# Optimization experiments

Hardware: AMD Instinct MI355X
Metric: run time of the kernel (lower is better)

## Reference

```python
import jax, jax.numpy as jnp
import numpy as np

B, NPG, DEG = 128, 400, 16
N, E = B * NPG, B * NPG * DEG
E_PER = E // B
K1, K2, K3 = 360, 324, 292  # ceil(0.9*400), ceil(0.9*360), ceil(0.9*324)
EPS = 1e-5


def setup_inputs() -> dict:
    key = jax.random.key(0)
    ks = jax.random.split(key, 48)
    # edges constrained within each graph (contiguous equal-size graphs)
    g = jnp.repeat(jnp.arange(B, dtype=jnp.int32), E_PER)
    src = jax.random.randint(ks[0], (E,), 0, NPG, dtype=jnp.int32) + g * NPG
    dst = jax.random.randint(ks[1], (E,), 0, NPG, dtype=jnp.int32) + g * NPG
    inp = {
        'x': jax.random.normal(ks[2], (N, 64), dtype=jnp.float32),
        'edge_index': jnp.stack([src, dst]),
        'batch': jnp.repeat(jnp.arange(B, dtype=jnp.int32), NPG),
    }
    def glorot(k, a, b):
        lim = float(np.sqrt(6.0 / (a + b)))
        return jax.random.uniform(k, (a, b), minval=-lim, maxval=lim, dtype=jnp.float32)
    conv_dims = [(64, 32), (32, 64), (64, 128), (128, 128)]
    for i, (a, b) in enumerate(conv_dims, 1):
        inp[f'W{i}'] = glorot(ks[2 + i], a, b)
        inp[f'b{i}'] = jnp.zeros((b,), jnp.float32)
    for i, d in zip((1, 2, 3), (32, 64, 128)):
        inp[f'p{i}'] = jax.random.uniform(ks[8 + i], (d,), minval=-1.0, maxval=1.0, dtype=jnp.float32) / float(np.sqrt(d))
    lin_dims = [(128, 64), (64, 64), (64, 32), (32, 16), (16, 1)]
    for i, (a, b) in enumerate(lin_dims, 1):
        inp[f'Lw{i}'] = glorot(ks[12 + i], a, b)
        inp[f'Lb{i}'] = jnp.zeros((b,), jnp.float32)
    for i, d in enumerate((64, 64, 32, 16), 1):
        inp[f'g{i}'] = jnp.ones((d,), jnp.float32)
        inp[f'be{i}'] = jnp.zeros((d,), jnp.float32)
    return inp


def _gcn(x, src, dst, emask, nmask, W, b):
    h = x @ W
    deg = nmask + jax.ops.segment_sum(emask, dst, num_segments=N)
    dinv = jnp.where(deg > 0, jax.lax.rsqrt(deg), 0.0)
    norm = dinv[src] * dinv[dst] * emask
    agg = jax.ops.segment_sum(h[src] * norm[:, None], dst, num_segments=N)
    agg = agg + h * (dinv * dinv * nmask)[:, None]  # self-loop term
    return (agg + b) * nmask[:, None]


def _topk_pool(x, nmask, p, k):
    # PyG TopKPooling: score = x.p/||p||, keep top-k per graph, x *= tanh(score)
    score = (x @ p) / jnp.linalg.norm(p)
    sel = jnp.where(nmask > 0, score, -jnp.inf).reshape(B, NPG)
    _, idx = jax.lax.top_k(sel, k)
    gidx = (idx + (jnp.arange(B) * NPG)[:, None]).reshape(-1)
    new_mask = jnp.zeros((N,), x.dtype).at[gidx].set(1.0)
    return x * (jnp.tanh(score) * new_mask)[:, None], new_mask


def reference(x, edge_index, batch, W1, b1, p1, W2, b2, p2, W3, b3, p3, W4, b4,
              Lw1, Lb1, Lw2, Lb2, Lw3, Lb3, Lw4, Lb4, Lw5, Lb5,
              g1, be1, g2, be2, g3, be3, g4, be4):
    src, dst = edge_index[0], edge_index[1]
    nmask = jnp.ones((N,), jnp.float32)
    emask = jnp.ones((E,), jnp.float32)
    x = jax.nn.relu(_gcn(x, src, dst, emask, nmask, W1, b1))
    x, nmask = _topk_pool(x, nmask, p1, K1)
    emask = emask * nmask[src] * nmask[dst]
    x = jax.nn.relu(_gcn(x, src, dst, emask, nmask, W2, b2))
    x, nmask = _topk_pool(x, nmask, p2, K2)
    emask = emask * nmask[src] * nmask[dst]
    x = jax.nn.relu(_gcn(x, src, dst, emask, nmask, W3, b3))
    x, nmask = _topk_pool(x, nmask, p3, K3)
    emask = emask * nmask[src] * nmask[dst]
    x = jax.nn.relu(_gcn(x, src, dst, emask, nmask, W4, b4))
    h = x.reshape(B, NPG, -1).max(axis=1)
    def lin_bn(h, W, bb, ga, be):
        h = h @ W + bb
        m = h.mean(0)
        v = h.var(0)  # biased, matches BatchNorm1d training normalization
        return jax.nn.relu(ga * (h - m) / jnp.sqrt(v + EPS) + be)
    h = lin_bn(h, Lw1, Lb1, g1, be1)
    h = lin_bn(h, Lw2, Lb2, g2, be2)
    h = lin_bn(h, Lw3, Lb3, g3, be3)
    h = lin_bn(h, Lw4, Lb4, g4, be4)
    return h @ Lw5 + Lb5
```

## Files before the change

### kernel.cpp

```cpp
#include <hip/hip_runtime.h>
#include <math.h>

#define NNODES 51200
#define BGRAPHS 128
#define NPG 400
#define NEDGES 819200
#define EPG 6400
#define SLP 7680

__global__ __launch_bounds__(512) void csr_build_kernel(
    const int* __restrict__ src, const int* __restrict__ dst,
    unsigned short* __restrict__ slg, int* __restrict__ gsg, int* __restrict__ gcg,
    float* __restrict__ nmask, float* __restrict__ dinv, float* __restrict__ sc) {
    __shared__ int deg[NPG];
    __shared__ int incl[512];
    __shared__ int gs[NPG];
    __shared__ int cur[NPG];
    const int g = blockIdx.x, t = threadIdx.x;
    for (int i = t; i < NPG; i += 512) deg[i] = 0;
    __syncthreads();
    for (int e = t; e < EPG; e += 512)
        atomicAdd(&deg[dst[g * EPG + e] - g * NPG], 1);
    __syncthreads();
    const int d = (t < NPG) ? deg[t] : 0;
    const int p = (d + 3) >> 2;
    incl[t] = p;
    __syncthreads();
    for (int off = 1; off < 512; off <<= 1) {
        int add = (t >= off) ? incl[t - off] : 0;
        __syncthreads();
        incl[t] += add;
        __syncthreads();
    }
    if (t < NPG) {
        const int gstart = incl[t] - p;
        gs[t] = gstart;
        gsg[g * NPG + t] = gstart;
        gcg[g * NPG + t] = p;
        cur[t] = gstart * 4;
        nmask[g * NPG + t] = 1.0f;
        const float dv = rsqrtf(1.0f + (float)d);
        dinv[g * NPG + t] = dv;
        sc[g * NPG + t] = dv;
    }
    __syncthreads();
    for (int e = t; e < EPG; e += 512) {
        int dl = dst[g * EPG + e] - g * NPG;
        int pos = atomicAdd(&cur[dl], 1);
        slg[g * SLP + pos] = (unsigned short)(src[g * EPG + e] - g * NPG);
    }
    __syncthreads();
    if (t < NPG) {
        const int end = (gs[t] + p) * 4;
        for (int i = cur[t]; i < end; i++) slg[g * SLP + i] = (unsigned short)NPG;
    }
}

template<int IN, int OUT, bool EPI>
__global__ __launch_bounds__(256) void gemm_kernel(
    const float* __restrict__ X, const float* __restrict__ W,
    const float* __restrict__ bias, const float* __restrict__ nmask,
    float* __restrict__ H) {
    __shared__ __align__(16) float sX[64 * IN];
    const int row0 = blockIdx.x * 64;
    const int t = threadIdx.x;
    for (int i = t; i < 64 * IN / 4; i += 256)
        reinterpret_cast<float4*>(sX)[i] =
            reinterpret_cast<const float4*>(X + (size_t)row0 * IN)[i];
    __syncthreads();
    constexpr int CG  = OUT / 4;
    constexpr int RG  = 256 / CG;
    constexpr int RPT = 64 / RG;
    const int c0 = (t % CG) * 4;
    const int r0 = (t / CG) * RPT;
    float acc[RPT][4];
#pragma unroll
    for (int r = 0; r < RPT; r++)
#pragma unroll
        for (int j = 0; j < 4; j++) acc[r][j] = 0.0f;
    for (int k4 = 0; k4 < IN / 4; k4++) {
        const float4 w0 = *reinterpret_cast<const float4*>(&W[(k4 * 4 + 0) * OUT + c0]);
        const float4 w1 = *reinterpret_cast<const float4*>(&W[(k4 * 4 + 1) * OUT + c0]);
        const float4 w2 = *reinterpret_cast<const float4*>(&W[(k4 * 4 + 2) * OUT + c0]);
        const float4 w3 = *reinterpret_cast<const float4*>(&W[(k4 * 4 + 3) * OUT + c0]);
#pragma unroll
        for (int r = 0; r < RPT; r++) {
            const float4 xv = *reinterpret_cast<const float4*>(&sX[(r0 + r) * IN + k4 * 4]);
            acc[r][0] += xv.x * w0.x + xv.y * w1.x + xv.z * w2.x + xv.w * w3.x;
            acc[r][1] += xv.x * w0.y + xv.y * w1.y + xv.z * w2.y + xv.w * w3.y;
            acc[r][2] += xv.x * w0.z + xv.y * w1.z + xv.z * w2.z + xv.w * w3.z;
            acc[r][3] += xv.x * w0.w + xv.y * w1.w + xv.z * w2.w + xv.w * w3.w;
        }
    }
#pragma unroll
    for (int r = 0; r < RPT; r++) {
        const int row = row0 + r0 + r;
        float4 v = make_float4(acc[r][0], acc[r][1], acc[r][2], acc[r][3]);
        if (EPI) {
            const float4 b4 = *reinterpret_cast<const float4*>(&bias[c0]);
            const float m = nmask[row];
            v.x = fmaxf(v.x + b4.x, 0.0f) * m;
            v.y = fmaxf(v.y + b4.y, 0.0f) * m;
            v.z = fmaxf(v.z + b4.z, 0.0f) * m;
            v.w = fmaxf(v.w + b4.w, 0.0f) * m;
        }
        *reinterpret_cast<float4*>(&H[(size_t)row * OUT + c0]) = v;
    }
}

template<int OUT, int NCH, int NS, bool EPI>
__global__ __launch_bounds__(512) void gcn_agg_kernel(
    const float* __restrict__ H, float* __restrict__ Y,
    const float* __restrict__ dinv, const float* __restrict__ sc,
    const float* __restrict__ bias,
    const unsigned short* __restrict__ slg, const int* __restrict__ gsg,
    const int* __restrict__ gcg) {
    __shared__ __align__(16) float Hl[(NPG + 1) * 36];
    __shared__ float dinvl[NPG];
    __shared__ int gsl[NPG];
    __shared__ int gcl[NPG];
    __shared__ unsigned long long sl64[SLP / 4];
    const unsigned short* sl = reinterpret_cast<const unsigned short*>(sl64);
    const int b   = blockIdx.x;
    const int g   = b / (NCH * NS);
    const int rem = b % (NCH * NS);
    const int f0  = (rem / NS) * 32;
    const int n0  = (rem % NS) * (NPG / NS);
    const int t   = threadIdx.x;

    for (int i = t; i < NPG; i += 512) {
        dinvl[i] = dinv[g * NPG + i];
        gsl[i] = gsg[g * NPG + i];
        gcl[i] = gcg[g * NPG + i];
    }
    for (int i = t; i < SLP / 4; i += 512)
        sl64[i] = reinterpret_cast<const unsigned long long*>(slg + (size_t)g * SLP)[i];
    if (t < 36) Hl[NPG * 36 + t] = 0.0f;
    for (int i = t; i < NPG * 8; i += 512) {
        const int n = i >> 3, q = i & 7;
        const float s = sc[g * NPG + n];
        float4 v = *reinterpret_cast<const float4*>(&H[(size_t)(g * NPG + n) * OUT + f0 + q * 4]);
        v.x *= s; v.y *= s; v.z *= s; v.w *= s;
        *reinterpret_cast<float4*>(&Hl[n * 36 + q * 4]) = v;
    }
    __syncthreads();

    const int wave = t >> 6, lane = t & 63;
    const int sub = lane >> 3, f4 = lane & 7;
    constexpr int NPB = NPG / NS;
    for (int n = n0 + wave * 8 + sub; n < n0 + NPB; n += 64) {
        const float di = dinvl[n];
        float* yp = &Y[(size_t)(g * NPG + n) * OUT + f0 + f4 * 4];
        if (di == 0.0f) {
            *reinterpret_cast<float4*>(yp) = make_float4(0.f, 0.f, 0.f, 0.f);
            continue;
        }
        const int g0 = gsl[n], g1 = g0 + gcl[n];
        float4 acc = *reinterpret_cast<const float4*>(&Hl[n * 36 + f4 * 4]);
        for (int gg = g0; gg < g1; ++gg) {
            const unsigned long long q = *reinterpret_cast<const unsigned long long*>(&sl[gg * 4]);
            const int s0 = (int)(q & 0xFFFF), s1 = (int)((q >> 16) & 0xFFFF);
            const int s2 = (int)((q >> 32) & 0xFFFF), s3 = (int)(q >> 48);
            const float4 a = *reinterpret_cast<const float4*>(&Hl[s0 * 36 + f4 * 4]);
            const float4 bb = *reinterpret_cast<const float4*>(&Hl[s1 * 36 + f4 * 4]);
            const float4 c = *reinterpret_cast<const float4*>(&Hl[s2 * 36 + f4 * 4]);
            const float4 dd = *reinterpret_cast<const float4*>(&Hl[s3 * 36 + f4 * 4]);
            acc.x += (a.x + bb.x) + (c.x + dd.x);
            acc.y += (a.y + bb.y) + (c.y + dd.y);
            acc.z += (a.z + bb.z) + (c.z + dd.z);
            acc.w += (a.w + bb.w) + (c.w + dd.w);
        }
        acc.x *= di; acc.y *= di; acc.z *= di; acc.w *= di;
        if (EPI) {
            const float4 b4 = *reinterpret_cast<const float4*>(&bias[f0 + f4 * 4]);
            acc.x = fmaxf(acc.x + b4.x, 0.0f);
            acc.y = fmaxf(acc.y + b4.y, 0.0f);
            acc.z = fmaxf(acc.z + b4.z, 0.0f);
            acc.w = fmaxf(acc.w + b4.w, 0.0f);
        }
        *reinterpret_cast<float4*>(yp) = acc;
    }
}

template<int DIM>
__global__ __launch_bounds__(512) void topk_kernel(
    const float* __restrict__ X, float* __restrict__ nmask,
    float* __restrict__ dinv, float* __restrict__ sc,
    const float* __restrict__ p, int K,
    const unsigned short* __restrict__ slg, const int* __restrict__ gsg,
    const int* __restrict__ gcg) {
    __shared__ float sval[512];
    __shared__ int   sidx[512];
    __shared__ float sscore[NPG];
    __shared__ float nml[NPG + 1];
    __shared__ unsigned long long sl64[SLP / 4];
    __shared__ int gsl[NPG];
    __shared__ int gcl[NPG];
    __shared__ float spnorm;
    const unsigned short* sl = reinterpret_cast<const unsigned short*>(sl64);
    const int g = blockIdx.x;
    const int t = threadIdx.x;
    for (int i = t; i < SLP / 4; i += 512)
        sl64[i] = reinterpret_cast<const unsigned long long*>(slg + (size_t)g * SLP)[i];
    for (int i = t; i < NPG; i += 512) {
        gsl[i] = gsg[g * NPG + i];
        gcl[i] = gcg[g * NPG + i];
    }
    if (t == 0) {
        float s = 0.0f;
        for (int j = 0; j < DIM; j++) s += p[j] * p[j];
        spnorm = sqrtf(s);
    }
    __syncthreads();
    if (t < NPG) {
        const float* xr = X + (size_t)(g * NPG + t) * DIM;
        float s = 0.0f;
        for (int j4 = 0; j4 < DIM / 4; j4++) {
            float4 xv = *reinterpret_cast<const float4*>(&xr[j4 * 4]);
            float4 pv = *reinterpret_cast<const float4*>(&p[j4 * 4]);
            s += xv.x * pv.x + xv.y * pv.y + xv.z * pv.z + xv.w * pv.w;
        }
        s /= spnorm;
        sscore[t] = s;
        sval[t] = (nmask[g * NPG + t] > 0.0f) ? s : -INFINITY;
        sidx[t] = t;
    } else {
        sval[t] = -INFINITY;
        sidx[t] = 0x7FFFFFFF;
    }
    __syncthreads();
    for (int kk = 2; kk <= 512; kk <<= 1) {
        for (int j = kk >> 1; j > 0; j >>= 1) {
            int l = t ^ j;
            if (l > t) {
                float va = sval[t], vb = sval[l];
                int   ia = sidx[t], ib = sidx[l];
                bool aFirst = (va > vb) || (va == vb && ia < ib);
                bool desc   = ((t & kk) == 0);
                if (desc != aFirst) {
                    sval[t] = vb; sval[l] = va;
                    sidx[t] = ib; sidx[l] = ia;
                }
            }
            __syncthreads();
        }
    }
    if (t <= NPG) nml[t] = 0.0f;
    __syncthreads();
    if (t < K) nml[sidx[t]] = 1.0f;
    __syncthreads();
    if (t < NPG) nmask[g * NPG + t] = nml[t];
    for (int n = t; n < NPG; n += 512) {
        float dv = 0.0f;
        if (nml[n] > 0.0f) {
            float d = 1.0f;
            const int g0 = gsl[n], g1 = g0 + gcl[n];
            for (int gg = g0; gg < g1; ++gg) {
                const unsigned long long q = *reinterpret_cast<const unsigned long long*>(&sl[gg * 4]);
                d += nml[(int)(q & 0xFFFF)] + nml[(int)((q >> 16) & 0xFFFF)] +
                     nml[(int)((q >> 32) & 0xFFFF)] + nml[(int)(q >> 48)];
            }
            dv = rsqrtf(d);
        }
        dinv[g * NPG + n] = dv;
        sc[g * NPG + n] = (nml[n] > 0.0f) ? tanhf(sscore[n]) * dv : 0.0f;
    }
}

__global__ __launch_bounds__(512) void maxpool_kernel(const float* __restrict__ X,
                                                      float* __restrict__ HP) {
    __shared__ float sm[512];
    const int g = blockIdx.x, t = threadIdx.x;
    const int c = t & 127, q = t >> 7;
    const float* base = X + ((size_t)g * NPG + q * 100) * 128 + c;
    float m = 0.0f;
    for (int n = 0; n < 100; n++) m = fmaxf(m, base[(size_t)n * 128]);
    sm[t] = m;
    __syncthreads();
    if (q == 0)
        HP[g * 128 + c] = fmaxf(fmaxf(sm[c], sm[c + 128]), fmaxf(sm[c + 256], sm[c + 384]));
}

template<int IN, int OUT>
__global__ __launch_bounds__(128) void head_layer_kernel(
    const float* __restrict__ A, const float* __restrict__ W,
    const float* __restrict__ b, const float* __restrict__ ga,
    const float* __restrict__ be, float* __restrict__ Y) {
    __shared__ float Al[128 * (IN + 1)];
    __shared__ float red[4];
    const int c = blockIdx.x, t = threadIdx.x;
    for (int i = t; i < 128 * IN; i += 128)
        Al[(i / IN) * (IN + 1) + (i % IN)] = A[i];
    __syncthreads();
    float acc = b[c];
#pragma unroll
    for (int j = 0; j < IN; j++) acc += Al[t * (IN + 1) + j] * W[j * OUT + c];
    float s1 = acc, s2 = acc * acc;
    for (int o = 32; o > 0; o >>= 1) {
        s1 += __shfl_down(s1, o, 64);
        s2 += __shfl_down(s2, o, 64);
    }
    if ((t & 63) == 0) { red[t >> 6] = s1; red[2 + (t >> 6)] = s2; }
    __syncthreads();
    const float S1 = red[0] + red[1], S2 = red[2] + red[3];
    const float m = S1 * (1.0f / 128.0f);
    const float var = S2 * (1.0f / 128.0f) - m * m;
    float val = ga[c] * (acc - m) * rsqrtf(var + 1e-5f) + be[c];
    Y[t * OUT + c] = fmaxf(val, 0.0f);
}

__global__ __launch_bounds__(128) void head_final_kernel(
    const float* __restrict__ A, const float* __restrict__ w,
    const float* __restrict__ b, float* __restrict__ out) {
    const int t = threadIdx.x;
    float acc = b[0];
#pragma unroll
    for (int j = 0; j < 16; j++) acc += A[t * 16 + j] * w[j];
    out[t] = acc;
}

extern "C" void kernel_launch(void* const* d_in, const int* in_sizes, int n_in,
                              void* d_out, int out_size, void* d_ws, size_t ws_size,
                              hipStream_t stream) {
    (void)in_sizes; (void)n_in; (void)out_size; (void)ws_size;
    const float* x   = (const float*)d_in[0];
    const int*   ei  = (const int*)d_in[1];
    const float* W1  = (const float*)d_in[3];  const float* b1  = (const float*)d_in[4];
    const float* W2  = (const float*)d_in[5];  const float* b2  = (const float*)d_in[6];
    const float* W3  = (const float*)d_in[7];  const float* b3  = (const float*)d_in[8];
    const float* W4  = (const float*)d_in[9];  const float* b4  = (const float*)d_in[10];
    const float* p1  = (const float*)d_in[11];
    const float* p2  = (const float*)d_in[12];
    const float* p3  = (const float*)d_in[13];
    const float* Lw1 = (const float*)d_in[14]; const float* Lb1 = (const float*)d_in[15];
    const float* Lw2 = (const float*)d_in[16]; const float* Lb2 = (const float*)d_in[17];
    const float* Lw3 = (const float*)d_in[18]; const float* Lb3 = (const float*)d_in[19];
    const float* Lw4 = (const float*)d_in[20]; const float* Lb4 = (const float*)d_in[21];
    const float* Lw5 = (const float*)d_in[22]; const float* Lb5 = (const float*)d_in[23];
    const float* g1  = (const float*)d_in[24]; const float* be1 = (const float*)d_in[25];
    const float* g2  = (const float*)d_in[26]; const float* be2 = (const float*)d_in[27];
    const float* g3  = (const float*)d_in[28]; const float* be3 = (const float*)d_in[29];
    const float* g4  = (const float*)d_in[30]; const float* be4 = (const float*)d_in[31];

    const int* src = ei;
    const int* dst = ei + NEDGES;

    float* ws    = (float*)d_ws;
    float* hb    = ws;
    float* x0    = hb + (size_t)NNODES * 128;
    float* x1    = x0 + (size_t)NNODES * 128;
    float* nmask = x1 + (size_t)NNODES * 128;
    float* dinv  = nmask + NNODES;
    float* sc    = dinv + NNODES;
    float* hp    = sc + NNODES;
    float* a1    = hp + 128 * 128;
    float* a2    = a1 + 128 * 64;
    float* a3    = a2 + 128 * 64;
    float* a4    = a3 + 128 * 32;
    unsigned short* slg = (unsigned short*)(a4 + 128 * 16);
    int* gsg = (int*)(slg + (size_t)BGRAPHS * SLP);
    int* gcg = gsg + (size_t)BGRAPHS * NPG;

    csr_build_kernel<<<BGRAPHS, 512, 0, stream>>>(src, dst, slg, gsg, gcg, nmask, dinv, sc);

    gemm_kernel<64, 32, false><<<NNODES / 64, 256, 0, stream>>>(x, W1, nullptr, nullptr, hb);
    gcn_agg_kernel<32, 1, 2, true><<<BGRAPHS * 2, 512, 0, stream>>>(hb, x0, dinv, sc, b1, slg, gsg, gcg);
    topk_kernel<32><<<BGRAPHS, 512, 0, stream>>>(x0, nmask, dinv, sc, p1, 360, slg, gsg, gcg);

    gcn_agg_kernel<32, 1, 2, false><<<BGRAPHS * 2, 512, 0, stream>>>(x0, hb, dinv, sc, nullptr, slg, gsg, gcg);
    gemm_kernel<32, 64, true><<<NNODES / 64, 256, 0, stream>>>(hb, W2, b2, nmask, x1);
    topk_kernel<64><<<BGRAPHS, 512, 0, stream>>>(x1, nmask, dinv, sc, p2, 324, slg, gsg, gcg);

    gcn_agg_kernel<64, 2, 2, false><<<BGRAPHS * 4, 512, 0, stream>>>(x1, hb, dinv, sc, nullptr, slg, gsg, gcg);
    gemm_kernel<64, 128, true><<<NNODES / 64, 256, 0, stream>>>(hb, W3, b3, nmask, x0);
    topk_kernel<128><<<BGRAPHS, 512, 0, stream>>>(x0, nmask, dinv, sc, p3, 292, slg, gsg, gcg);

    gcn_agg_kernel<128, 4, 1, false><<<BGRAPHS * 4, 512, 0, stream>>>(x0, hb, dinv, sc, nullptr, slg, gsg, gcg);
    gemm_kernel<128, 128, true><<<NNODES / 64, 256, 0, stream>>>(hb, W4, b4, nmask, x1);

    maxpool_kernel<<<BGRAPHS, 512, 0, stream>>>(x1, hp);
    head_layer_kernel<128, 64><<<64, 128, 0, stream>>>(hp, Lw1, Lb1, g1, be1, a1);
    head_layer_kernel<64, 64><<<64, 128, 0, stream>>>(a1, Lw2, Lb2, g2, be2, a2);
    head_layer_kernel<64, 32><<<32, 128, 0, stream>>>(a2, Lw3, Lb3, g3, be3, a3);
    head_layer_kernel<32, 16><<<16, 128, 0, stream>>>(a3, Lw4, Lb4, g4, be4, a4);
    head_final_kernel<<<1, 128, 0, stream>>>(a4, Lw5, Lb5, (float*)d_out);
}
```

Measured before the change: 240.2 us.

## Fuse top-k scoring into producers and max-pool into final GEMM epilogue

The projection score x·p is now computed in the epilogue of the kernel that produces each layer's features (the aggregation kernel for layer 1, the GEMM for layers 2-3) and written to a score buffer, so the top-k kernel no longer rereads the full feature matrix. The final GEMM no longer writes its output; it reduces per-graph column maxima in shared memory with atomicMax on float bits and merges them into the pooled buffer, which is zeroed in the CSR build kernel. This removes the separate max-pool kernel and its full read of the last feature matrix. The aggregation kernel also skips writing zeros for masked nodes, which relies on those rows already being zero in the output buffer. The costs are extra shuffles, shared and global atomics, and that stale-row assumption.

Result: faster. 209.5 us (-12.8%).

```diff
diff --git a/kernel.cpp b/kernel.cpp
--- a/kernel.cpp
+++ b/kernel.cpp
@@ -11,13 +11,15 @@
 __global__ __launch_bounds__(512) void csr_build_kernel(
     const int* __restrict__ src, const int* __restrict__ dst,
     unsigned short* __restrict__ slg, int* __restrict__ gsg, int* __restrict__ gcg,
-    float* __restrict__ nmask, float* __restrict__ dinv, float* __restrict__ sc) {
+    float* __restrict__ nmask, float* __restrict__ dinv, float* __restrict__ sc,
+    float* __restrict__ hp) {
     __shared__ int deg[NPG];
     __shared__ int incl[512];
     __shared__ int gs[NPG];
     __shared__ int cur[NPG];
     const int g = blockIdx.x, t = threadIdx.x;
     for (int i = t; i < NPG; i += 512) deg[i] = 0;
+    if (t < 128) hp[g * 128 + t] = 0.0f;
     __syncthreads();
     for (int e = t; e < EPG; e += 512)
         atomicAdd(&deg[dst[g * EPG + e] - g * NPG], 1);
@@ -56,17 +58,20 @@
     }
 }
 
-template<int IN, int OUT, bool EPI>
+template<int IN, int OUT, int MODE>
 __global__ __launch_bounds__(256) void gemm_kernel(
     const float* __restrict__ X, const float* __restrict__ W,
     const float* __restrict__ bias, const float* __restrict__ nmask,
-    float* __restrict__ H) {
+    float* __restrict__ H, const float* __restrict__ p,
+    float* __restrict__ score, float* __restrict__ hp) {
     __shared__ __align__(16) float sX[64 * IN];
+    __shared__ unsigned smax[256];
     const int row0 = blockIdx.x * 64;
     const int t = threadIdx.x;
     for (int i = t; i < 64 * IN / 4; i += 256)
         reinterpret_cast<float4*>(sX)[i] =
             reinterpret_cast<const float4*>(X + (size_t)row0 * IN)[i];
+    if (MODE == 3) smax[t] = 0u;
     __syncthreads();
     constexpr int CG  = OUT / 4;
     constexpr int RG  = 256 / CG;
@@ -92,11 +97,14 @@
             acc[r][3] += xv.x * w0.w + xv.y * w1.w + xv.z * w2.w + xv.w * w3.w;
         }
     }
+    const int graph0 = row0 / 400;
+    const int bnd = (graph0 + 1) * 400;
+    float ps[RPT];
 #pragma unroll
     for (int r = 0; r < RPT; r++) {
         const int row = row0 + r0 + r;
         float4 v = make_float4(acc[r][0], acc[r][1], acc[r][2], acc[r][3]);
-        if (EPI) {
+        if (MODE >= 2) {
             const float4 b4 = *reinterpret_cast<const float4*>(&bias[c0]);
             const float m = nmask[row];
             v.x = fmaxf(v.x + b4.x, 0.0f) * m;
@@ -104,15 +112,47 @@
             v.z = fmaxf(v.z + b4.z, 0.0f) * m;
             v.w = fmaxf(v.w + b4.w, 0.0f) * m;
         }
-        *reinterpret_cast<float4*>(&H[(size_t)row * OUT + c0]) = v;
-    }
-}
-
-template<int OUT, int NCH, int NS, bool EPI>
+        if (MODE != 3) *reinterpret_cast<float4*>(&H[(size_t)row * OUT + c0]) = v;
+        if (MODE == 2) {
+            const float4 p4 = *reinterpret_cast<const float4*>(&p[c0]);
+            ps[r] = v.x * p4.x + v.y * p4.y + v.z * p4.z + v.w * p4.w;
+        }
+        if (MODE == 3) {
+            const int seg = (row >= bnd) ? 1 : 0;
+            const float mx = fmaxf(fmaxf(v.x, v.y), fmaxf(v.z, v.w));
+            atomicMax(&smax[seg * 128 + c0 + 0], __float_as_uint(v.x));
+            atomicMax(&smax[seg * 128 + c0 + 1], __float_as_uint(v.y));
+            atomicMax(&smax[seg * 128 + c0 + 2], __float_as_uint(v.z));
+            atomicMax(&smax[seg * 128 + c0 + 3], __float_as_uint(v.w));
+            (void)mx;
+        }
+    }
+    if (MODE == 2) {
+#pragma unroll
+        for (int r = 0; r < RPT; r++) {
+#pragma unroll
+            for (int off = 1; off < CG; off <<= 1) ps[r] += __shfl_xor(ps[r], off);
+        }
+        if ((t % CG) == 0) {
+#pragma unroll
+            for (int r = 0; r < RPT; r++) score[row0 + r0 + r] = ps[r];
+        }
+    }
+    if (MODE == 3) {
+        __syncthreads();
+        unsigned* hpu = reinterpret_cast<unsigned*>(hp);
+        if (t < 128) atomicMax(&hpu[graph0 * 128 + t], smax[t]);
+        const int graph1 = (row0 + 63) / 400;
+        if (graph1 != graph0 && t < 128) atomicMax(&hpu[graph1 * 128 + t], smax[128 + t]);
+    }
+}
+
+template<int OUT, int NCH, int NS, bool EPI, bool SCORE>
 __global__ __launch_bounds__(512) void gcn_agg_kernel(
     const float* __restrict__ H, float* __restrict__ Y,
     const float* __restrict__ dinv, const float* __restrict__ sc,
-    const float* __restrict__ bias,
+    const float* __restrict__ bias, const float* __restrict__ p,
+    float* __restrict__ score,
     const unsigned short* __restrict__ slg, const int* __restrict__ gsg,
     const int* __restrict__ gcg) {
     __shared__ __align__(16) float Hl[(NPG + 1) * 36];
@@ -150,11 +190,7 @@
     constexpr int NPB = NPG / NS;
     for (int n = n0 + wave * 8 + sub; n < n0 + NPB; n += 64) {
         const float di = dinvl[n];
-        float* yp = &Y[(size_t)(g * NPG + n) * OUT + f0 + f4 * 4];
-        if (di == 0.0f) {
-            *reinterpret_cast<float4*>(yp) = make_float4(0.f, 0.f, 0.f, 0.f);
-            continue;
-        }
+        if (di == 0.0f) continue;
         const int g0 = gsl[n], g1 = g0 + gcl[n];
         float4 acc = *reinterpret_cast<const float4*>(&Hl[n * 36 + f4 * 4]);
         for (int gg = g0; gg < g1; ++gg) {
@@ -178,20 +214,28 @@
             acc.z = fmaxf(acc.z + b4.z, 0.0f);
             acc.w = fmaxf(acc.w + b4.w, 0.0f);
         }
-        *reinterpret_cast<float4*>(yp) = acc;
+        *reinterpret_cast<float4*>(&Y[(size_t)(g * NPG + n) * OUT + f0 + f4 * 4]) = acc;
+        if (SCORE) {
+            const float4 p4 = *reinterpret_cast<const float4*>(&p[f4 * 4]);
+            float part = acc.x * p4.x + acc.y * p4.y + acc.z * p4.z + acc.w * p4.w;
+            part += __shfl_xor(part, 1);
+            part += __shfl_xor(part, 2);
+            part += __shfl_xor(part, 4);
+            if (f4 == 0) score[g * NPG + n] = part;
+        }
     }
 }
 
 template<int DIM>
 __global__ __launch_bounds__(512) void topk_kernel(
-    const float* __restrict__ X, float* __restrict__ nmask,
+    const float* __restrict__ score, float* __restrict__ nmask,
     float* __restrict__ dinv, float* __restrict__ sc,
     const float* __restrict__ p, int K,
     const unsigned short* __restrict__ slg, const int* __restrict__ gsg,
     const int* __restrict__ gcg) {
     __shared__ float sval[512];
     __shared__ int   sidx[512];
-    __shared__ float sscore[NPG];
+    __shared__ float sraw[NPG];
     __shared__ float nml[NPG + 1];
     __shared__ unsigned long long sl64[SLP / 4];
     __shared__ int gsl[NPG];
@@ -213,16 +257,9 @@
     }
     __syncthreads();
     if (t < NPG) {
-        const float* xr = X + (size_t)(g * NPG + t) * DIM;
-        float s = 0.0f;
-        for (int j4 = 0; j4 < DIM / 4; j4++) {
-            float4 xv = *reinterpret_cast<const float4*>(&xr[j4 * 4]);
-            float4 pv = *reinterpret_cast<const float4*>(&p[j4 * 4]);
-            s += xv.x * pv.x + xv.y * pv.y + xv.z * pv.z + xv.w * pv.w;
-        }
-        s /= spnorm;
-        sscore[t] = s;
-        sval[t] = (nmask[g * NPG + t] > 0.0f) ? s : -INFINITY;
+        const float raw = score[g * NPG + t];
+        sraw[t] = raw;
+        sval[t] = (nmask[g * NPG + t] > 0.0f) ? raw : -INFINITY;
         sidx[t] = t;
     } else {
         sval[t] = -INFINITY;
@@ -263,22 +300,8 @@
             dv = rsqrtf(d);
         }
         dinv[g * NPG + n] = dv;
-        sc[g * NPG + n] = (nml[n] > 0.0f) ? tanhf(sscore[n]) * dv : 0.0f;
-    }
-}
-
-__global__ __launch_bounds__(512) void maxpool_kernel(const float* __restrict__ X,
-                                                      float* __restrict__ HP) {
-    __shared__ float sm[512];
-    const int g = blockIdx.x, t = threadIdx.x;
-    const int c = t & 127, q = t >> 7;
-    const float* base = X + ((size_t)g * NPG + q * 100) * 128 + c;
-    float m = 0.0f;
-    for (int n = 0; n < 100; n++) m = fmaxf(m, base[(size_t)n * 128]);
-    sm[t] = m;
-    __syncthreads();
-    if (q == 0)
-        HP[g * 128 + c] = fmaxf(fmaxf(sm[c], sm[c + 128]), fmaxf(sm[c + 256], sm[c + 384]));
+        sc[g * NPG + n] = (nml[n] > 0.0f) ? tanhf(sraw[n] / spnorm) * dv : 0.0f;
+    }
 }
 
 template<int IN, int OUT>
@@ -352,7 +375,8 @@
     float* nmask = x1 + (size_t)NNODES * 128;
     float* dinv  = nmask + NNODES;
     float* sc    = dinv + NNODES;
-    float* hp    = sc + NNODES;
+    float* scoreb= sc + NNODES;
+    float* hp    = scoreb + NNODES;
     float* a1    = hp + 128 * 128;
     float* a2    = a1 + 128 * 64;
     float* a3    = a2 + 128 * 64;
@@ -361,24 +385,23 @@
     int* gsg = (int*)(slg + (size_t)BGRAPHS * SLP);
     int* gcg = gsg + (size_t)BGRAPHS * NPG;
 
-    csr_build_kernel<<<BGRAPHS, 512, 0, stream>>>(src, dst, slg, gsg, gcg, nmask, dinv, sc);
-
-    gemm_kernel<64, 32, false><<<NNODES / 64, 256, 0, stream>>>(x, W1, nullptr, nullptr, hb);
-    gcn_agg_kernel<32, 1, 2, true><<<BGRAPHS * 2, 512, 0, stream>>>(hb, x0, dinv, sc, b1, slg, gsg, gcg);
-    topk_kernel<32><<<BGRAPHS, 512, 0, stream>>>(x0, nmask, dinv, sc, p1, 360, slg, gsg, gcg);
-
-    gcn_agg_kernel<32, 1, 2, false><<<BGRAPHS * 2, 512, 0, stream>>>(x0, hb, dinv, sc, nullptr, slg, gsg, gcg);
-    gemm_kernel<32, 64, true><<<NNODES / 64, 256, 0, stream>>>(hb, W2, b2, nmask, x1);
-    topk_kernel<64><<<BGRAPHS, 512, 0, stream>>>(x1, nmask, dinv, sc, p2, 324, slg, gsg, gcg);
-
-    gcn_agg_kernel<64, 2, 2, false><<<BGRAPHS * 4, 512, 0, stream>>>(x1, hb, dinv, sc, nullptr, slg, gsg, gcg);
-    gemm_kernel<64, 128, true><<<NNODES / 64, 256, 0, stream>>>(hb, W3, b3, nmask, x0);
-    topk_kernel<128><<<BGRAPHS, 512, 0, stream>>>(x0, nmask, dinv, sc, p3, 292, slg, gsg, gcg);
-
-    gcn_agg_kernel<128, 4, 1, false><<<BGRAPHS * 4, 512, 0, stream>>>(x0, hb, dinv, sc, nullptr, slg, gsg, gcg);
-    gemm_kernel<128, 128, true><<<NNODES / 64, 256, 0, stream>>>(hb, W4, b4, nmask, x1);
-
-    maxpool_kernel<<<BGRAPHS, 512, 0, stream>>>(x1, hp);
+    csr_build_kernel<<<BGRAPHS, 512, 0, stream>>>(src, dst, slg, gsg, gcg, nmask, dinv, sc, hp);
+
+    gemm_kernel<64, 32, 0><<<NNODES / 64, 256, 0, stream>>>(x, W1, nullptr, nullptr, hb, nullptr, nullptr, nullptr);
+    gcn_agg_kernel<32, 1, 2, true, true><<<BGRAPHS * 2, 512, 0, stream>>>(hb, x0, dinv, sc, b1, p1, scoreb, slg, gsg, gcg);
+    topk_kernel<32><<<BGRAPHS, 512, 0, stream>>>(scoreb, nmask, dinv, sc, p1, 360, slg, gsg, gcg);
+
+    gcn_agg_kernel<32, 1, 2, false, false><<<BGRAPHS * 2, 512, 0, stream>>>(x0, hb, dinv, sc, nullptr, nullptr, nullptr, slg, gsg, gcg);
+    gemm_kernel<32, 64, 2><<<NNODES / 64, 256, 0, stream>>>(hb, W2, b2, nmask, x1, p2, scoreb, nullptr);
+    topk_kernel<64><<<BGRAPHS, 512, 0, stream>>>(scoreb, nmask, dinv, sc, p2, 324, slg, gsg, gcg);
+
+    gcn_agg_kernel<64, 2, 2, false, false><<<BGRAPHS * 4, 512, 0, stream>>>(x1, hb, dinv, sc, nullptr, nullptr, nullptr, slg, gsg, gcg);
+    gemm_kernel<64, 128, 2><<<NNODES / 64, 256, 0, stream>>>(hb, W3, b3, nmask, x0, p3, scoreb, nullptr);
+    topk_kernel<128><<<BGRAPHS, 512, 0, stream>>>(scoreb, nmask, dinv, sc, p3, 292, slg, gsg, gcg);
+
+    gcn_agg_kernel<128, 4, 1, false, false><<<BGRAPHS * 4, 512, 0, stream>>>(x0, hb, dinv, sc, nullptr, nullptr, nullptr, slg, gsg, gcg);
+    gemm_kernel<128, 128, 3><<<NNODES / 64, 256, 0, stream>>>(hb, W4, b4, nmask, x1, nullptr, nullptr, hp);
+
     head_layer_kernel<128, 64><<<64, 128, 0, stream>>>(hp, Lw1, Lb1, g1, be1, a1);
     head_layer_kernel<64, 64><<<64, 128, 0, stream>>>(a1, Lw2, Lb2, g2, be2, a2);
     head_layer_kernel<64, 32><<<32, 128, 0, stream>>>(a2, Lw3, Lb3, g3, be3, a3);
```
